# Optimization experiments

Hardware: AMD Instinct MI355X
Metric: run time of the kernel (lower is better)

## Reference

```python
import jax, jax.numpy as jnp
import numpy as np

N_E, E_DIM, BETA = 8192, 512, 0.25


def setup_inputs() -> dict:
    key = jax.random.key(0)
    k1, k2 = jax.random.split(key)
    z = jax.random.normal(k1, (16, 1024, E_DIM), dtype=jnp.float32)
    # embedding initialized uniform(-1/n_e, 1/n_e)
    emb_w = jax.random.uniform(k2, (N_E, E_DIM), dtype=jnp.float32,
                               minval=-1.0 / N_E, maxval=1.0 / N_E)
    return {"z": z, "emb_w": emb_w}


def reference(z, emb_w):
    B, T, D = z.shape
    zf = z.reshape(-1, D)  # [BT, D]
    # squared-distance matrix: ||z||^2 + ||e||^2 - 2 z e^T  -> [BT, n_e]
    d = (jnp.sum(zf * zf, axis=1, keepdims=True)
         + jnp.sum(emb_w * emb_w, axis=1)
         - 2.0 * jnp.einsum('bd,nd->bn', zf, emb_w))
    idx = jnp.argmin(d, axis=1)  # [BT]
    z_q = emb_w[idx].reshape(z.shape)  # [B, T, D]
    # legacy=False: beta * commit + codebook term
    loss = (BETA * jnp.mean((jax.lax.stop_gradient(z_q) - z) ** 2)
            + jnp.mean((z_q - jax.lax.stop_gradient(z)) ** 2))
    # straight-through: value equals z_q
    z_q_st = z + jax.lax.stop_gradient(z_q - z)
    idx_out = idx.reshape(B, T)
    v = jnp.var(idx_out.astype(jnp.float32))
    return z_q_st, loss, idx_out, v
```

## Files before the change

### kernel.cpp

```cpp
#include <hip/hip_runtime.h>


#define BT   16384
#define DIMS 512
#define NE   8192
#define NS   4
#define BN   256
#define NTPB (NE / NS / BN)
#define NSTEPS 64

#define LOSS_OFF 8388608
#define IDX_OFF  8388609
#define V_OFF    8404993

#define BEST_OFF  0
#define ENORM_OFF 131072
#define SUMS_OFF  163840
#define CNT_OFF   163864

typedef __attribute__((ext_vector_type(8))) short short8;
typedef __attribute__((ext_vector_type(4))) float floatx4;

#define AS1(p) ((const __attribute__((address_space(1))) void*)(p))
#define AS3(p) ((__attribute__((address_space(3))) void*)(p))

__device__ __forceinline__ unsigned f2bf(float f) {
    unsigned u = __builtin_bit_cast(unsigned, f);
    u += 0x7FFFu + ((u >> 16) & 1u);
    return u >> 16;
}

__global__ __launch_bounds__(256) void prep_kernel(
    const float* __restrict__ z, const float* __restrict__ emb,
    ushort* __restrict__ zh, ushort* __restrict__ ehh,
    float* __restrict__ enorm, unsigned long long* __restrict__ best,
    double* __restrict__ sums, unsigned* __restrict__ counter)
{
    const int lane = threadIdx.x & 63, w = threadIdx.x >> 6;
    const int b = blockIdx.x;
    if (b < NE / 4) {
        const int row = b * 4 + w;
        const float4* p = (const float4*)(emb + (size_t)row * DIMS + lane * 8);
        float4 a = p[0], bb = p[1];
        uint4 h;
        h.x = f2bf(a.x) | (f2bf(a.y) << 16);
        h.y = f2bf(a.z) | (f2bf(a.w) << 16);
        h.z = f2bf(bb.x) | (f2bf(bb.y) << 16);
        h.w = f2bf(bb.z) | (f2bf(bb.w) << 16);
        *(uint4*)(ehh + (size_t)row * DIMS + lane * 8) = h;
        float s = a.x*a.x + a.y*a.y + a.z*a.z + a.w*a.w
                + bb.x*bb.x + bb.y*bb.y + bb.z*bb.z + bb.w*bb.w;
        #pragma unroll
        for (int off = 32; off > 0; off >>= 1) s += __shfl_down(s, off, 64);
        if (lane == 0) enorm[row] = s;
    } else {
        const int row = (b - NE / 4) * 4 + w;
        const float4* p = (const float4*)(z + (size_t)row * DIMS + lane * 8);
        float4 a = p[0], bb = p[1];
        uint4 h;
        h.x = f2bf(a.x) | (f2bf(a.y) << 16);
        h.y = f2bf(a.z) | (f2bf(a.w) << 16);
        h.z = f2bf(bb.x) | (f2bf(bb.y) << 16);
        h.w = f2bf(bb.z) | (f2bf(bb.w) << 16);
        *(uint4*)(zh + (size_t)row * DIMS + lane * 8) = h;
    }
    const int gid = b * 256 + threadIdx.x;
    if (gid < BT) best[gid] = 0xFFFFFFFFFFFFFFFFULL;
    if (gid == 0) { sums[0] = 0.0; sums[1] = 0.0; sums[2] = 0.0; *counter = 0u; }
}


#define PIN __builtin_amdgcn_sched_barrier(0)
#define P1  __builtin_amdgcn_s_setprio(1)
#define P0  __builtin_amdgcn_s_setprio(0)

#define DSR8O(dst, BASE, OFF) \
    asm volatile("ds_read_b128 %0, %1 offset:" #OFF : "=v"(dst) : "v"(BASE))

#define LGK(N_) do {                                                           \
    asm volatile("s_waitcnt lgkmcnt(" #N_ ")" ::: "memory");                   \
    __builtin_amdgcn_sched_barrier(0);                                         \
} while (0)

#define CL4(J_, BIDX_, KK_)                                                    \
    _Pragma("unroll")                                                          \
    for (int mi = 0; mi < 4; mi++)                                             \
        acc[mi][J_] = __builtin_amdgcn_mfma_f32_16x16x32_bf16(                 \
            a[mi][KK_], b[BIDX_], acc[mi][J_], 0, 0, 0);

#define STAGE_A(SA_, H_, DST_) do {                                            \
    const int sc_ = (SA_) & 63;                                                \
    const unsigned al_ = (DST_) + (unsigned)((((H_) * 128) + w * 8) * 64);     \
    const ushort* g_ = zA + (size_t)((H_) * 128) * DIMS + soff                 \
                     + ((sc_ & 7) * 64);                                       \
    __builtin_amdgcn_global_load_lds(AS1(g_), AS3(&lds[al_]), 16, 0, 0);       \
    __builtin_amdgcn_global_load_lds(AS1(g_ + (size_t)64 * DIMS),              \
                                     AS3(&lds[al_ + 4096]), 16, 0, 0);         \
} while (0)

#define STAGE_B(SB_, H_, DST_) do {                                            \
    const int sc_ = (SB_) & 63;                                                \
    const unsigned bl_ = (DST_) + (unsigned)((((H_) * 128) + w * 8) * 64);     \
    const ushort* g_ = eh + (size_t)(nsN + (sc_ >> 3) * 256 + (H_) * 128) * DIMS \
                     + soff + ((sc_ & 7) * 64);                                \
    __builtin_amdgcn_global_load_lds(AS1(g_), AS3(&lds[bl_]), 16, 0, 0);       \
    __builtin_amdgcn_global_load_lds(AS1(g_ + (size_t)64 * DIMS),              \
                                     AS3(&lds[bl_ + 4096]), 16, 0, 0);         \
} while (0)

#define STEP(S_, AR_, BR_, AW_, BW_, TM_) do {                                 \
    const int s_ = (S_);                                                       \
    short8 a[4][2], b[4];                                                      \
    const unsigned aV0 = ldsb + 2u * ((AR_) + aro + pxo0);                     \
    const unsigned aV1 = ldsb + 2u * ((AR_) + aro + pxo1);                     \
    const unsigned bV0 = ldsb + 2u * ((BR_) + bro + pxo0);                     \
    const unsigned bV1 = ldsb + 2u * ((BR_) + bro + pxo1);                     \
    DSR8O(a[0][0], aV0, 0);    DSR8O(a[1][0], aV0, 2048);                      \
    DSR8O(a[2][0], aV0, 4096); DSR8O(a[3][0], aV0, 6144);                      \
    DSR8O(b[0], bV0, 0);       DSR8O(b[1], bV0, 2048);                         \
    DSR8O(b[2], bV0, 4096);    DSR8O(b[3], bV0, 6144);                         \
    DSR8O(a[0][1], aV1, 0);    DSR8O(a[1][1], aV1, 2048);                      \
    DSR8O(a[2][1], aV1, 4096); DSR8O(a[3][1], aV1, 6144);                      \
    STAGE_B(s_ + 1, 0, BW_); STAGE_B(s_ + 1, 1, BW_);                          \
    STAGE_A(s_ + 2, 0, AW_); STAGE_A(s_ + 2, 1, AW_);                          \
    LGK(7); P1; CL4(0, 0, 0); PIN; P0; DSR8O(b[0], bV0, 8192);                 \
    LGK(7); P1; CL4(1, 1, 0); PIN; P0; DSR8O(b[1], bV0, 10240);                \
    LGK(7); P1; CL4(2, 2, 0); PIN; P0; DSR8O(b[2], bV0, 12288);                \
    LGK(7); P1; CL4(3, 3, 0); PIN; P0; DSR8O(b[3], bV0, 14336);                \
    LGK(3); P1; CL4(4, 0, 0); PIN; P0; DSR8O(b[0], bV1, 0);                    \
    LGK(3); P1; CL4(5, 1, 0); PIN; P0; DSR8O(b[1], bV1, 2048);                 \
    LGK(3); P1; CL4(6, 2, 0); PIN; P0; DSR8O(b[2], bV1, 4096);                 \
    LGK(3); P1; CL4(7, 3, 0); PIN; P0; DSR8O(b[3], bV1, 6144);                 \
    LGK(3); P1; CL4(0, 0, 1); PIN; P0; DSR8O(b[0], bV1, 8192);                 \
    LGK(3); P1; CL4(1, 1, 1); PIN; P0; DSR8O(b[1], bV1, 10240);                \
    LGK(3); P1; CL4(2, 2, 1); PIN; P0; DSR8O(b[2], bV1, 12288);                \
    LGK(3); P1; CL4(3, 3, 1); PIN; P0; DSR8O(b[3], bV1, 14336);                \
    LGK(3); P1; CL4(4, 0, 1); PIN; P0;                                         \
    LGK(2); P1; CL4(5, 1, 1); PIN; P0;                                         \
    LGK(1); P1; CL4(6, 2, 1); PIN; P0;                                         \
    LGK(0); P1; CL4(7, 3, 1); PIN; P0;                                         \
    if ((TM_) == 0) asm volatile("s_waitcnt vmcnt(4)" ::: "memory");           \
    __builtin_amdgcn_s_barrier();                                              \
} while (0)

__global__ __launch_bounds__(512, 2) void argmin_mfma(
    const ushort* __restrict__ zh, const ushort* __restrict__ eh,
    const float* __restrict__ enorm, unsigned long long* __restrict__ best)
{
    __shared__ __align__(16) ushort lds[81920];

    const int t = threadIdx.x;
    const int w = t >> 6, lane = t & 63;
    const int quad = lane >> 4, l15 = lane & 15;

    const int d = blockIdx.x;
    const int xcd = d & 7, slot = d >> 3;
    const int ns = xcd >> 1;
    const int mt = slot * 2 + (xcd & 1);
    const int m0 = mt * 256;
    const int nsN = ns * (NTPB * BN);

    const int wrow = (w & 3) * 64;
    const int wcol = (w >> 2) * 128;

    const int l8 = lane >> 3, c8 = lane & 7;
    const int chunk = c8 ^ l8;
    const int soff = (w * 8 + l8) * DIMS + chunk * 8;
    const ushort* zA = zh + (size_t)m0 * DIMS;
    const float* enormg = enorm + nsN;

    const int pxo0 = (quad ^ (l15 & 7)) * 8;
    const int pxo1 = ((4 + quad) ^ (l15 & 7)) * 8;
    const int aro = (wrow + l15) * 64;
    const int bro = (wcol + l15) * 64;
    const unsigned ldsb = (unsigned)(size_t)AS3(&lds[0]);

    floatx4 acc[4][8];
    #pragma unroll
    for (int mi = 0; mi < 4; mi++)
        #pragma unroll
        for (int nj = 0; nj < 8; nj++)
            acc[mi][nj] = (floatx4){0.f, 0.f, 0.f, 0.f};

    float bs[16];
    int   bn_[16];
    #pragma unroll
    for (int k = 0; k < 16; k++) { bs[k] = 3.4e38f; bn_[k] = 0; }

    STAGE_A(0, 0, 0u);     STAGE_A(0, 1, 0u);
    STAGE_B(0, 0, 49152u); STAGE_B(0, 1, 49152u);
    STAGE_A(1, 0, 16384u); STAGE_A(1, 1, 16384u);
    asm volatile("s_waitcnt vmcnt(4)" ::: "memory");
    __builtin_amdgcn_s_barrier();

    unsigned aR = 0u, aN = 16384u, aW = 32768u;

    for (int sp = 0; sp < NSTEPS; sp += 2) {
        STEP(sp, aR, 49152u, aW, 65536u, 0);
        { unsigned t_ = aR; aR = aN; aN = aW; aW = t_; }
        STEP(sp + 1, aR, 65536u, aW, 49152u, (sp == NSTEPS - 2) ? 2 : 0);
        { unsigned t_ = aR; aR = aN; aN = aW; aW = t_; }

        if ((sp & 7) == 6) {
            const int nt = sp >> 3;
            const int eb = nt * 256 + wcol + l15;
            const int nbase = nsN + eb;
            float en[8];
            #pragma unroll
            for (int nj = 0; nj < 8; nj++) {
                const float* ep_ = enormg + eb + nj * 16;
                asm volatile("global_load_dword %0, %1, off"
                             : "=v"(en[nj]) : "v"(ep_));
            }
            asm volatile("s_waitcnt vmcnt(0)" ::: "memory");
            __builtin_amdgcn_sched_barrier(0);
            #pragma unroll
            for (int nj = 0; nj < 8; nj++) {
                const int n = nbase + nj * 16;
                #pragma unroll
                for (int mi = 0; mi < 4; mi++) {
                    #pragma unroll
                    for (int r = 0; r < 4; r++) {
                        const int k = mi * 4 + r;
                        const float sc = fmaf(-2.0f, acc[mi][nj][r], en[nj]);
                        if (sc < bs[k]) { bs[k] = sc; bn_[k] = n; }
                    }
                    acc[mi][nj] = (floatx4){0.f, 0.f, 0.f, 0.f};
                }
            }
        }
    }

    asm volatile("s_waitcnt vmcnt(0)" ::: "memory");

    #pragma unroll
    for (int mi = 0; mi < 4; mi++)
        #pragma unroll
        for (int r = 0; r < 4; r++) {
            const int k = mi * 4 + r;
            unsigned su = __builtin_bit_cast(unsigned, bs[k]);
            su = (su & 0x80000000u) ? ~su : (su | 0x80000000u);
            unsigned long long key = ((unsigned long long)su << 32) | (unsigned)bn_[k];
            #pragma unroll
            for (int off = 1; off < 16; off <<= 1) {
                unsigned long long o = __shfl_xor(key, off, 64);
                key = (o < key) ? o : key;
            }
            if (l15 == 0) atomicMin(&best[m0 + wrow + mi * 16 + quad * 4 + r], key);
        }
}

__global__ __launch_bounds__(256) void gather_loss_kernel(
    const float* __restrict__ z, const float* __restrict__ emb,
    const unsigned long long* __restrict__ best,
    float* __restrict__ out, double* __restrict__ sums, unsigned* __restrict__ counter)
{
    __shared__ int sIdx[32];
    __shared__ double red[4];
    const int t = threadIdx.x;
    const int row0 = blockIdx.x * 32;
    double myIdxSum = 0.0, myIdxSq = 0.0;
    if (t < 32) {
        int row = row0 + t;
        int idx = (int)(unsigned)(best[row] & 0xFFFFFFFFULL);
        sIdx[t] = idx;
        out[IDX_OFF + row] = (float)idx;
        myIdxSum = (double)idx;
        myIdxSq = (double)idx * (double)idx;
    }
    __syncthreads();
    double acc = 0.0;
    #pragma unroll 4
    for (int i = 0; i < 16; i++) {
        int e = i * 1024 + t * 4;
        int rl = e >> 9;
        int c = e & 511;
        int idx = sIdx[rl];
        float4 zv = *(const float4*)(z + (size_t)(row0 + rl) * DIMS + c);
        float4 ev = *(const float4*)(emb + (size_t)idx * DIMS + c);
        *(float4*)(out + (size_t)(row0 + rl) * DIMS + c) = ev;
        float dx = zv.x - ev.x, dy = zv.y - ev.y;
        float dz = zv.z - ev.z, dw = zv.w - ev.w;
        acc += (double)(dx * dx + dy * dy) + (double)(dz * dz + dw * dw);
    }
    const int lane = t & 63, wv = t >> 6;
    #pragma unroll
    for (int off = 32; off > 0; off >>= 1) {
        acc      += __shfl_down(acc, off, 64);
        myIdxSum += __shfl_down(myIdxSum, off, 64);
        myIdxSq  += __shfl_down(myIdxSq, off, 64);
    }
    if (lane == 0) red[wv] = acc;
    __syncthreads();
    if (t == 0) {
        double tot = red[0] + red[1] + red[2] + red[3];
        atomicAdd(&sums[0], tot);
        atomicAdd(&sums[1], myIdxSum);
        atomicAdd(&sums[2], myIdxSq);
        __threadfence();
        unsigned old = atomicAdd(counter, 1u);
        if (old == gridDim.x - 1) {
            __threadfence();
            double s0 = atomicAdd(&sums[0], 0.0);
            double s1 = atomicAdd(&sums[1], 0.0);
            double s2 = atomicAdd(&sums[2], 0.0);
            out[LOSS_OFF] = (float)(1.25 * s0 / (double)((size_t)BT * DIMS));
            double m = s1 / (double)BT;
            out[V_OFF] = (float)(s2 / (double)BT - m * m);
        }
    }
}

extern "C" void kernel_launch(void* const* d_in, const int* in_sizes, int n_in,
                              void* d_out, int out_size, void* d_ws, size_t ws_size,
                              hipStream_t stream) {
    const float* z = (const float*)d_in[0];
    const float* emb = (const float*)d_in[1];
    float* out = (float*)d_out;
    char* ws = (char*)d_ws;
    unsigned long long* best = (unsigned long long*)(ws + BEST_OFF);
    float* enorm  = (float*)(ws + ENORM_OFF);
    double* sums  = (double*)(ws + SUMS_OFF);
    unsigned* counter = (unsigned*)(ws + CNT_OFF);

    ushort* zh = (ushort*)out;
    ushort* ehh = zh + (size_t)BT * DIMS;

    hipLaunchKernelGGL(prep_kernel, dim3(NE / 4 + BT / 4), dim3(256), 0, stream,
                       z, emb, zh, ehh, enorm, best, sums, counter);
    hipLaunchKernelGGL(argmin_mfma, dim3(256), dim3(512), 0, stream,
                       zh, ehh, enorm, best);
    hipLaunchKernelGGL(gather_loss_kernel, dim3(BT / 32), dim3(256), 0, stream,
                       z, emb, best, out, sums, counter);
}
```

Measured before the change: 248.2 us.

## Retile argmin GEMM to 256x128 blocks with 4 waves and BK=32

Reshapes the distance/argmin MFMA kernel from 512-thread blocks computing 256x256 tiles over 4 codebook splits into 256-thread blocks computing 256x128 tiles over 8 splits, with a K-step of 32 instead of 64. LDS use shrinks from 160KB to 64KB, the swizzle and staging are rewritten for 32-wide rows, and the MFMA/ds_read interleave is simplified. The aim is higher occupancy and more blocks (512) for better CU fill and latency hiding. The cost is lower arithmetic intensity per block, twice as many barriers and K-steps, and more global traffic for the z tile, which is re-read across twice as many codebook splits.

Measured after the change: 287.0 us. +15.6%, slower.

```diff
diff --git a/kernel.cpp b/kernel.cpp
--- a/kernel.cpp
+++ b/kernel.cpp
@@ -4,10 +4,10 @@
 #define BT   16384
 #define DIMS 512
 #define NE   8192
-#define NS   4
-#define BN   256
+#define NS   8
+#define BN   128
 #define NTPB (NE / NS / BN)
-#define NSTEPS 64
+#define NSTEPS 128
 
 #define LOSS_OFF 8388608
 #define IDX_OFF  8388609
@@ -70,10 +70,6 @@
 }
 
 
-#define PIN __builtin_amdgcn_sched_barrier(0)
-#define P1  __builtin_amdgcn_s_setprio(1)
-#define P0  __builtin_amdgcn_s_setprio(0)
-
 #define DSR8O(dst, BASE, OFF) \
     asm volatile("ds_read_b128 %0, %1 offset:" #OFF : "=v"(dst) : "v"(BASE))
 
@@ -82,97 +78,80 @@
     __builtin_amdgcn_sched_barrier(0);                                         \
 } while (0)
 
-#define CL4(J_, BIDX_, KK_)                                                    \
+#define CL4(J_, BIDX_)                                                         \
     _Pragma("unroll")                                                          \
     for (int mi = 0; mi < 4; mi++)                                             \
         acc[mi][J_] = __builtin_amdgcn_mfma_f32_16x16x32_bf16(                 \
-            a[mi][KK_], b[BIDX_], acc[mi][J_], 0, 0, 0);
+            a[mi], b[BIDX_], acc[mi][J_], 0, 0, 0);
 
 #define STAGE_A(SA_, H_, DST_) do {                                            \
-    const int sc_ = (SA_) & 63;                                                \
-    const unsigned al_ = (DST_) + (unsigned)((((H_) * 128) + w * 8) * 64);     \
-    const ushort* g_ = zA + (size_t)((H_) * 128) * DIMS + soff                 \
-                     + ((sc_ & 7) * 64);                                       \
+    const int sc_ = (SA_) & (NSTEPS - 1);                                      \
+    const int rb_ = ((H_) * 4 + w) * 16;                                       \
+    const unsigned al_ = (DST_) + (unsigned)(rb_ * 32);                        \
+    const ushort* g_ = zA + (size_t)rb_ * DIMS + soff + ((sc_ & 15) * 32);     \
     __builtin_amdgcn_global_load_lds(AS1(g_), AS3(&lds[al_]), 16, 0, 0);       \
-    __builtin_amdgcn_global_load_lds(AS1(g_ + (size_t)64 * DIMS),              \
-                                     AS3(&lds[al_ + 4096]), 16, 0, 0);         \
 } while (0)
 
 #define STAGE_B(SB_, H_, DST_) do {                                            \
-    const int sc_ = (SB_) & 63;                                                \
-    const unsigned bl_ = (DST_) + (unsigned)((((H_) * 128) + w * 8) * 64);     \
-    const ushort* g_ = eh + (size_t)(nsN + (sc_ >> 3) * 256 + (H_) * 128) * DIMS \
-                     + soff + ((sc_ & 7) * 64);                                \
+    const int sc_ = (SB_) & (NSTEPS - 1);                                      \
+    const int rb_ = ((H_) * 4 + w) * 16;                                       \
+    const unsigned bl_ = (DST_) + (unsigned)(rb_ * 32);                        \
+    const ushort* g_ = eh + (size_t)(nsN + (sc_ >> 4) * BN + rb_) * DIMS       \
+                     + soff + ((sc_ & 15) * 32);                               \
     __builtin_amdgcn_global_load_lds(AS1(g_), AS3(&lds[bl_]), 16, 0, 0);       \
-    __builtin_amdgcn_global_load_lds(AS1(g_ + (size_t)64 * DIMS),              \
-                                     AS3(&lds[bl_ + 4096]), 16, 0, 0);         \
 } while (0)
 
 #define STEP(S_, AR_, BR_, AW_, BW_, TM_) do {                                 \
     const int s_ = (S_);                                                       \
-    short8 a[4][2], b[4];                                                      \
-    const unsigned aV0 = ldsb + 2u * ((AR_) + aro + pxo0);                     \
-    const unsigned aV1 = ldsb + 2u * ((AR_) + aro + pxo1);                     \
-    const unsigned bV0 = ldsb + 2u * ((BR_) + bro + pxo0);                     \
-    const unsigned bV1 = ldsb + 2u * ((BR_) + bro + pxo1);                     \
-    DSR8O(a[0][0], aV0, 0);    DSR8O(a[1][0], aV0, 2048);                      \
-    DSR8O(a[2][0], aV0, 4096); DSR8O(a[3][0], aV0, 6144);                      \
-    DSR8O(b[0], bV0, 0);       DSR8O(b[1], bV0, 2048);                         \
-    DSR8O(b[2], bV0, 4096);    DSR8O(b[3], bV0, 6144);                         \
-    DSR8O(a[0][1], aV1, 0);    DSR8O(a[1][1], aV1, 2048);                      \
-    DSR8O(a[2][1], aV1, 4096); DSR8O(a[3][1], aV1, 6144);                      \
+    short8 a[4], b[8];                                                         \
+    const unsigned aV = ldsb + 2u * ((AR_) + aro + pxo);                       \
+    const unsigned bV = ldsb + 2u * ((BR_) + bro + pxo);                       \
+    DSR8O(a[0], aV, 0);    DSR8O(a[1], aV, 1024);                              \
+    DSR8O(a[2], aV, 2048); DSR8O(a[3], aV, 3072);                              \
+    DSR8O(b[0], bV, 0);    DSR8O(b[1], bV, 1024);                              \
+    DSR8O(b[2], bV, 2048); DSR8O(b[3], bV, 3072);                              \
+    DSR8O(b[4], bV, 4096); DSR8O(b[5], bV, 5120);                              \
+    DSR8O(b[6], bV, 6144); DSR8O(b[7], bV, 7168);                              \
     STAGE_B(s_ + 1, 0, BW_); STAGE_B(s_ + 1, 1, BW_);                          \
     STAGE_A(s_ + 2, 0, AW_); STAGE_A(s_ + 2, 1, AW_);                          \
-    LGK(7); P1; CL4(0, 0, 0); PIN; P0; DSR8O(b[0], bV0, 8192);                 \
-    LGK(7); P1; CL4(1, 1, 0); PIN; P0; DSR8O(b[1], bV0, 10240);                \
-    LGK(7); P1; CL4(2, 2, 0); PIN; P0; DSR8O(b[2], bV0, 12288);                \
-    LGK(7); P1; CL4(3, 3, 0); PIN; P0; DSR8O(b[3], bV0, 14336);                \
-    LGK(3); P1; CL4(4, 0, 0); PIN; P0; DSR8O(b[0], bV1, 0);                    \
-    LGK(3); P1; CL4(5, 1, 0); PIN; P0; DSR8O(b[1], bV1, 2048);                 \
-    LGK(3); P1; CL4(6, 2, 0); PIN; P0; DSR8O(b[2], bV1, 4096);                 \
-    LGK(3); P1; CL4(7, 3, 0); PIN; P0; DSR8O(b[3], bV1, 6144);                 \
-    LGK(3); P1; CL4(0, 0, 1); PIN; P0; DSR8O(b[0], bV1, 8192);                 \
-    LGK(3); P1; CL4(1, 1, 1); PIN; P0; DSR8O(b[1], bV1, 10240);                \
-    LGK(3); P1; CL4(2, 2, 1); PIN; P0; DSR8O(b[2], bV1, 12288);                \
-    LGK(3); P1; CL4(3, 3, 1); PIN; P0; DSR8O(b[3], bV1, 14336);                \
-    LGK(3); P1; CL4(4, 0, 1); PIN; P0;                                         \
-    LGK(2); P1; CL4(5, 1, 1); PIN; P0;                                         \
-    LGK(1); P1; CL4(6, 2, 1); PIN; P0;                                         \
-    LGK(0); P1; CL4(7, 3, 1); PIN; P0;                                         \
+    STAGE_A(s_ + 2, 2, AW_); STAGE_A(s_ + 2, 3, AW_);                          \
+    __builtin_amdgcn_s_setprio(1);                                             \
+    LGK(7); CL4(0, 0); LGK(6); CL4(1, 1); LGK(5); CL4(2, 2); LGK(4); CL4(3, 3);\
+    LGK(3); CL4(4, 4); LGK(2); CL4(5, 5); LGK(1); CL4(6, 6); LGK(0); CL4(7, 7);\
+    __builtin_amdgcn_s_setprio(0);                                             \
+    __builtin_amdgcn_sched_barrier(0);                                         \
     if ((TM_) == 0) asm volatile("s_waitcnt vmcnt(4)" ::: "memory");           \
     __builtin_amdgcn_s_barrier();                                              \
 } while (0)
 
-__global__ __launch_bounds__(512, 2) void argmin_mfma(
+__global__ __launch_bounds__(256, 2) void argmin_mfma(
     const ushort* __restrict__ zh, const ushort* __restrict__ eh,
     const float* __restrict__ enorm, unsigned long long* __restrict__ best)
 {
-    __shared__ __align__(16) ushort lds[81920];
+    __shared__ __align__(16) ushort lds[32768];
 
     const int t = threadIdx.x;
     const int w = t >> 6, lane = t & 63;
     const int quad = lane >> 4, l15 = lane & 15;
 
     const int d = blockIdx.x;
-    const int xcd = d & 7, slot = d >> 3;
-    const int ns = xcd >> 1;
-    const int mt = slot * 2 + (xcd & 1);
+    const int xcd = d & 7;
+    const int ns = xcd;
+    const int mt = d >> 3;
     const int m0 = mt * 256;
     const int nsN = ns * (NTPB * BN);
 
-    const int wrow = (w & 3) * 64;
-    const int wcol = (w >> 2) * 128;
-
-    const int l8 = lane >> 3, c8 = lane & 7;
-    const int chunk = c8 ^ l8;
-    const int soff = (w * 8 + l8) * DIMS + chunk * 8;
+    const int wrow = w * 64;
+
+    const int lr = lane >> 2, lc = lane & 3;
+    const int clog = lc ^ (lr & 3);
+    const int soff = lr * DIMS + clog * 8;
     const ushort* zA = zh + (size_t)m0 * DIMS;
     const float* enormg = enorm + nsN;
 
-    const int pxo0 = (quad ^ (l15 & 7)) * 8;
-    const int pxo1 = ((4 + quad) ^ (l15 & 7)) * 8;
-    const int aro = (wrow + l15) * 64;
-    const int bro = (wcol + l15) * 64;
+    const int pxo = (quad ^ (l15 & 3)) * 8;
+    const int aro = (wrow + l15) * 32;
+    const int bro = l15 * 32;
     const unsigned ldsb = (unsigned)(size_t)AS3(&lds[0]);
 
     floatx4 acc[4][8];
@@ -187,23 +166,24 @@
     #pragma unroll
     for (int k = 0; k < 16; k++) { bs[k] = 3.4e38f; bn_[k] = 0; }
 
-    STAGE_A(0, 0, 0u);     STAGE_A(0, 1, 0u);
-    STAGE_B(0, 0, 49152u); STAGE_B(0, 1, 49152u);
-    STAGE_A(1, 0, 16384u); STAGE_A(1, 1, 16384u);
+    STAGE_A(0, 0, 0u); STAGE_A(0, 1, 0u); STAGE_A(0, 2, 0u); STAGE_A(0, 3, 0u);
+    STAGE_B(0, 0, 24576u); STAGE_B(0, 1, 24576u);
+    STAGE_A(1, 0, 8192u); STAGE_A(1, 1, 8192u);
+    STAGE_A(1, 2, 8192u); STAGE_A(1, 3, 8192u);
     asm volatile("s_waitcnt vmcnt(4)" ::: "memory");
     __builtin_amdgcn_s_barrier();
 
-    unsigned aR = 0u, aN = 16384u, aW = 32768u;
+    unsigned aR = 0u, aN = 8192u, aW = 16384u;
 
     for (int sp = 0; sp < NSTEPS; sp += 2) {
-        STEP(sp, aR, 49152u, aW, 65536u, 0);
+        STEP(sp, aR, 24576u, aW, 28672u, 0);
         { unsigned t_ = aR; aR = aN; aN = aW; aW = t_; }
-        STEP(sp + 1, aR, 65536u, aW, 49152u, (sp == NSTEPS - 2) ? 2 : 0);
+        STEP(sp + 1, aR, 28672u, aW, 24576u, (sp == NSTEPS - 2) ? 2 : 0);
         { unsigned t_ = aR; aR = aN; aN = aW; aW = t_; }
 
-        if ((sp & 7) == 6) {
-            const int nt = sp >> 3;
-            const int eb = nt * 256 + wcol + l15;
+        if ((sp & 15) == 14) {
+            const int nt = sp >> 4;
+            const int eb = nt * BN + l15;
             const int nbase = nsN + eb;
             float en[8];
             #pragma unroll
@@ -328,7 +308,7 @@
 
     hipLaunchKernelGGL(prep_kernel, dim3(NE / 4 + BT / 4), dim3(256), 0, stream,
                        z, emb, zh, ehh, enorm, best, sums, counter);
-    hipLaunchKernelGGL(argmin_mfma, dim3(256), dim3(512), 0, stream,
+    hipLaunchKernelGGL(argmin_mfma, dim3(512), dim3(256), 0, stream,
                        zh, ehh, enorm, best);
     hipLaunchKernelGGL(gather_loss_kernel, dim3(BT / 32), dim3(256), 0, stream,
                        z, emb, best, out, sums, counter);
```
